# Kernel tuning notes

Hardware: AMD Instinct MI355X
Metric: run time of the kernel (lower is better)

Reference implementation:

```python
import jax, jax.numpy as jnp
import numpy as np

N_NODES = 100000
N_EDGES = 800000
DIM = 64
HEADS = 4
HEAD_DIM = DIM // HEADS  # 16
ALPHA = 0.1
K_ITERS = 8  # fixed-point iterations approximating the implicit/CG solve


def setup_inputs() -> dict:
    key = jax.random.key(0)
    ks = jax.random.split(key, 7)
    x = jax.random.normal(ks[0], (N_NODES, DIM), dtype=jnp.float32)
    edge_index = jax.random.randint(ks[1], (2, N_EDGES), 0, N_NODES, dtype=jnp.int64)
    edge_attr = jax.random.normal(ks[2], (N_EDGES, DIM), dtype=jnp.float32)
    s = 1.0 / np.sqrt(DIM)
    Wq = jax.random.normal(ks[3], (DIM, DIM), dtype=jnp.float32) * s
    Wk = jax.random.normal(ks[4], (DIM, DIM), dtype=jnp.float32) * s
    Wv = jax.random.normal(ks[5], (DIM, DIM), dtype=jnp.float32) * s
    We = jax.random.normal(ks[6], (DIM, DIM), dtype=jnp.float32) * s
    return {"x": x, "edge_index": edge_index, "edge_attr": edge_attr,
            "Wq": Wq, "Wk": Wk, "Wv": Wv, "We": We}


def _mapr(x, edge_index, edge_attr, Wq, Wk, Wv, We):
    N = x.shape[0]
    src, dst = edge_index[0], edge_index[1]
    q = (x @ Wq).reshape(N, HEADS, HEAD_DIM)
    k = (x @ Wk).reshape(N, HEADS, HEAD_DIM)
    v = (x @ Wv).reshape(N, HEADS, HEAD_DIM)
    e = (edge_attr @ We).reshape(-1, HEADS, HEAD_DIM)
    # per-edge multi-head dot attention logits, edge features modulate keys
    logits = jnp.sum(q[dst] * (k[src] + e), axis=-1) / np.sqrt(HEAD_DIM)  # [E,H]
    # segment softmax over incoming edges of each dst node
    m = jax.ops.segment_max(logits, dst, num_segments=N)  # [N,H]
    ex = jnp.exp(logits - m[dst])
    denom = jax.ops.segment_sum(ex, dst, num_segments=N)  # [N,H]
    att = ex / (denom[dst] + 1e-16)  # [E,H]
    # implicit propagation: fixed-point solve of z = alpha*v + (1-alpha) * A_att z
    def step(z, _):
        msg = att[:, :, None] * z[src]                       # [E,H,D]
        agg = jax.ops.segment_sum(msg, dst, num_segments=N)  # [N,H,D]
        return ALPHA * v + (1.0 - ALPHA) * agg, None
    z, _ = jax.lax.scan(step, v, None, length=K_ITERS)
    return z.reshape(N, DIM)


def reference(x, edge_index, edge_attr, Wq, Wk, Wv, We):
    h = _mapr(x, edge_index, edge_attr, Wq, Wk, Wv, We)
    h = jax.nn.relu(h)  # act; dropout is identity in eval mode
    return x + h        # residual
```

## Files before the change

kernel.cpp:

```cpp
#include <hip/hip_runtime.h>
#include <hip/hip_fp16.h>
#include <cstdint>
#include <cstddef>

#define NN 100000
#define NE 800000
#define DIM 64
#define HEADS 4
#define HEAD_DIM 16
#define ALPHA 0.1f
#define K_ITERS 8
#define NBLK 391

typedef short bf16x8 __attribute__((ext_vector_type(8)));
typedef float f32x4 __attribute__((ext_vector_type(4)));
typedef float fvec4 __attribute__((ext_vector_type(4)));

__device__ __forceinline__ unsigned short f2bf(float f) {
    unsigned int x = __float_as_uint(f);
    unsigned int r = (x + 0x7fffu + ((x >> 16) & 1u)) >> 16;
    return (unsigned short)r;
}
__device__ __forceinline__ float bf_lo(unsigned int p) { return __uint_as_float(p << 16); }
__device__ __forceinline__ float bf_hi(unsigned int p) { return __uint_as_float(p & 0xffff0000u); }

__device__ __forceinline__ float2 h2f(unsigned int v) {
    __half2 h = *(__half2*)&v;
    return __half22float2(h);
}
__device__ __forceinline__ unsigned int f2h2(float a, float b) {
    __half2 h = __floats2half2_rn(a, b);
    return *(unsigned int*)&h;
}
__device__ __forceinline__ float dot8h(uint4 a, uint4 b) {
    float2 a0 = h2f(a.x), b0 = h2f(b.x);
    float2 a1 = h2f(a.y), b1 = h2f(b.y);
    float2 a2 = h2f(a.z), b2 = h2f(b.z);
    float2 a3 = h2f(a.w), b3 = h2f(b.w);
    return a0.x * b0.x + a0.y * b0.y + a1.x * b1.x + a1.y * b1.y
         + a2.x * b2.x + a2.y * b2.y + a3.x * b3.x + a3.y * b3.y;
}

#define ACC8(a, V) { float2 t_; \
    t_ = h2f((V).x); m[0] += (a) * t_.x; m[1] += (a) * t_.y; \
    t_ = h2f((V).y); m[2] += (a) * t_.x; m[3] += (a) * t_.y; \
    t_ = h2f((V).z); m[4] += (a) * t_.x; m[5] += (a) * t_.y; \
    t_ = h2f((V).w); m[6] += (a) * t_.x; m[7] += (a) * t_.y; }

__device__ __forceinline__ float rec_att(uint4 r, int head) {
    unsigned int pair = (head & 2) ? r.z : r.y;
    float2 f = h2f(pair);
    return (head & 1) ? f.y : f.x;
}

__global__ __launch_bounds__(256) void qkv_mfma_kernel(
    const float* __restrict__ x,
    const float* __restrict__ Wq, const float* __restrict__ Wk,
    const float* __restrict__ Wv, const float* __restrict__ We,
    __half* __restrict__ qh, __half* __restrict__ kh, __half* __restrict__ vh,
    unsigned short* __restrict__ u)
{
    __shared__ unsigned short sq[64 * 72];
    int tid = threadIdx.x;
    int w = tid >> 6;
    int lane = tid & 63;
    int m16 = lane & 15;
    int quad = lane >> 4;
    int node = blockIdx.x * 64 + w * 16 + m16;
    int nodeC = node < NN ? node : NN - 1;

    bf16x8 afrag[2];
    #pragma unroll
    for (int kk = 0; kk < 2; ++kk) {
        const float* xr = x + (size_t)nodeC * DIM + kk * 32 + quad * 8;
        #pragma unroll
        for (int j = 0; j < 8; ++j) afrag[kk][j] = (short)f2bf(xr[j]);
    }

    const float* Ws[3] = {Wq, Wk, Wv};
    __half* outs[3] = {qh, kh, vh};

    #pragma unroll
    for (int mtx = 0; mtx < 3; ++mtx) {
        const float* W = Ws[mtx];
        #pragma unroll
        for (int n0 = 0; n0 < 64; n0 += 16) {
            int col = n0 + m16;
            f32x4 acc = {0.f, 0.f, 0.f, 0.f};
            #pragma unroll
            for (int kk = 0; kk < 2; ++kk) {
                bf16x8 bfrag;
                #pragma unroll
                for (int j = 0; j < 8; ++j)
                    bfrag[j] = (short)f2bf(W[(kk * 32 + quad * 8 + j) * DIM + col]);
                acc = __builtin_amdgcn_mfma_f32_16x16x32_bf16(afrag[kk], bfrag, acc, 0, 0, 0);
            }
            if (mtx == 0) {
                #pragma unroll
                for (int r = 0; r < 4; ++r) acc[r] *= 0.25f;
            }
            #pragma unroll
            for (int r = 0; r < 4; ++r) {
                int rl = w * 16 + quad * 4 + r;
                int gnode = blockIdx.x * 64 + rl;
                if (mtx == 0) sq[rl * 72 + col] = f2bf(acc[r]);
                if (gnode < NN) outs[mtx][(size_t)gnode * DIM + col] = __float2half(acc[r]);
            }
        }
    }
    __syncthreads();

    #pragma unroll
    for (int h = 0; h < HEADS; ++h) {
        int kk = h >> 1;
        bf16x8 aq;
        const unsigned short* sr = &sq[(w * 16 + m16) * 72 + kk * 32 + quad * 8];
        #pragma unroll
        for (int j = 0; j < 8; ++j) aq[j] = (short)sr[j];
        #pragma unroll
        for (int c0 = 0; c0 < 64; c0 += 16) {
            int c = c0 + m16;
            bf16x8 bfrag;
            #pragma unroll
            for (int j = 0; j < 8; ++j) {
                int k = kk * 32 + quad * 8 + j;
                bfrag[j] = ((k >> 4) == h) ? (short)f2bf(We[c * DIM + k]) : (short)0;
            }
            f32x4 acc = {0.f, 0.f, 0.f, 0.f};
            acc = __builtin_amdgcn_mfma_f32_16x16x32_bf16(aq, bfrag, acc, 0, 0, 0);
            #pragma unroll
            for (int r = 0; r < 4; ++r) {
                int gnode = blockIdx.x * 64 + w * 16 + quad * 4 + r;
                if (gnode < NN) u[(size_t)gnode * 256 + h * 64 + c] = f2bf(acc[r]);
            }
        }
    }
}

__global__ void init_kernel(int* __restrict__ deg) {
    int i = blockIdx.x * 256 + threadIdx.x;
    if (i < NN) deg[i] = 0;
}

__global__ void deg_kernel(const int* __restrict__ ei, int* __restrict__ deg) {
    int e = blockIdx.x * 256 + threadIdx.x;
    if (e >= NE) return;
    atomicAdd(&deg[ei[NE + e]], 1);
}

__global__ void blocksum_kernel(const int* __restrict__ deg, int* __restrict__ bsum) {
    int t = threadIdx.x, b = blockIdx.x;
    int idx = b * 256 + t;
    int v = (idx < NN) ? deg[idx] : 0;
    #pragma unroll
    for (int off = 32; off > 0; off >>= 1) v += __shfl_down(v, off);
    __shared__ int wsum[4];
    if ((t & 63) == 0) wsum[t >> 6] = v;
    __syncthreads();
    if (t == 0) bsum[b] = wsum[0] + wsum[1] + wsum[2] + wsum[3];
}

__global__ void bscan_kernel(const int* __restrict__ bsum, int* __restrict__ boff) {
    __shared__ int s[512];
    int t = threadIdx.x;
    int v = (t < NBLK) ? bsum[t] : 0;
    s[t] = v;
    __syncthreads();
    for (int off = 1; off < 512; off <<= 1) {
        int u = (t >= off) ? s[t - off] : 0;
        __syncthreads();
        s[t] += u;
        __syncthreads();
    }
    if (t < NBLK) boff[t] = s[t] - v;
}

__global__ void rowptr_kernel(const int* __restrict__ deg, const int* __restrict__ boff,
                              int* __restrict__ row_ptr, int* __restrict__ cursor) {
    __shared__ int s[256];
    int t = threadIdx.x, b = blockIdx.x;
    int idx = b * 256 + t;
    int v = (idx < NN) ? deg[idx] : 0;
    s[t] = v;
    __syncthreads();
    for (int off = 1; off < 256; off <<= 1) {
        int u = (t >= off) ? s[t - off] : 0;
        __syncthreads();
        s[t] += u;
        __syncthreads();
    }
    if (idx < NN) {
        int ex = boff[b] + s[t] - v;
        row_ptr[idx] = ex;
        cursor[idx] = ex;
    }
    if (idx == 0) row_ptr[NN] = NE;
}

__global__ void scatter_kernel(const int* __restrict__ ei,
                               int* __restrict__ cursor,
                               int* __restrict__ csr_src,
                               int* __restrict__ csr_e,
                               int* __restrict__ csr_dst) {
    int e = blockIdx.x * 256 + threadIdx.x;
    if (e >= NE) return;
    int src = ei[e], dst = ei[NE + e];
    int pos = atomicAdd(&cursor[dst], 1);
    csr_src[pos] = src;
    csr_e[pos] = e;
    csr_dst[pos] = dst;
}

__global__ __launch_bounds__(256) void logits_edge_kernel(
    const __half* __restrict__ qh,
    const __half* __restrict__ kh,
    const float* __restrict__ edge_attr,
    const unsigned short* __restrict__ u,
    const int* __restrict__ ei,
    __half* __restrict__ att_e) {
    int idx = blockIdx.x * 256 + threadIdx.x;
    if (idx >= NE * HEADS) return;
    int e = idx >> 2, h = idx & 3;
    int src = ei[e], dst = ei[NE + e];
    const fvec4* attr4 = (const fvec4*)edge_attr + (size_t)e * 16;
    const uint4* u4 = (const uint4*)u + (size_t)dst * 32 + h * 8;
    float au = 0.f;
    #pragma unroll
    for (int i = 0; i < 8; ++i) {
        uint4 up = u4[i];
        fvec4 a0 = __builtin_nontemporal_load(attr4 + 2 * i);
        fvec4 a1 = __builtin_nontemporal_load(attr4 + 2 * i + 1);
        au += a0.x * bf_lo(up.x) + a0.y * bf_hi(up.x)
            + a0.z * bf_lo(up.y) + a0.w * bf_hi(up.y)
            + a1.x * bf_lo(up.z) + a1.y * bf_hi(up.z)
            + a1.z * bf_lo(up.w) + a1.w * bf_hi(up.w);
    }
    const uint4* qq = (const uint4*)qh + (size_t)dst * 8 + h * 2;
    const uint4* kk = (const uint4*)kh + (size_t)src * 8 + h * 2;
    float qk = dot8h(qq[0], kk[0]) + dot8h(qq[1], kk[1]);
    float ex = __expf(qk + au);
    att_e[idx] = __float2half(ex);
}

__global__ void rinv_kernel(const __half* __restrict__ att_e,
                            const int* __restrict__ csr_e,
                            const int* __restrict__ row_ptr,
                            float* __restrict__ rinv) {
    int idx = blockIdx.x * 256 + threadIdx.x;
    if (idx >= NN * HEADS) return;
    int n = idx >> 2, h = idx & 3;
    int beg = row_ptr[n], end = row_ptr[n + 1];
    float s = 0.f;
    int j = beg;
    for (; j + 2 <= end; j += 2) {
        int e0 = csr_e[j], e1 = csr_e[j + 1];
        float a0 = __half2float(att_e[e0 * 4 + h]);
        float a1 = __half2float(att_e[e1 * 4 + h]);
        s += a0 + a1;
    }
    if (j < end) s += __half2float(att_e[csr_e[j] * 4 + h]);
    rinv[idx] = 0.9f / (s + 1e-16f);
}

__global__ void recs_kernel(const __half* __restrict__ att_e,
                            const int* __restrict__ csr_src,
                            const int* __restrict__ csr_e,
                            const int* __restrict__ csr_dst,
                            const float* __restrict__ rinv,
                            uint4* __restrict__ recs) {
    int j = blockIdx.x * 256 + threadIdx.x;
    if (j >= NE) return;
    int e = csr_e[j], src = csr_src[j], dst = csr_dst[j];
    uint2 ap = *(const uint2*)(att_e + (size_t)e * 4);
    float2 e01 = h2f(ap.x), e23 = h2f(ap.y);
    float4 rv = *(const float4*)(rinv + (size_t)dst * 4);
    uint4 rec;
    rec.x = (unsigned int)src;
    rec.y = f2h2(e01.x * rv.x, e01.y * rv.y);
    rec.z = f2h2(e23.x * rv.z, e23.y * rv.w);
    rec.w = 0u;
    recs[j] = rec;
}

__global__ __launch_bounds__(256) void prop_rec_kernel(
    const __half* __restrict__ zin,
    const __half* __restrict__ vh,
    const uint4* __restrict__ recs,
    const int* __restrict__ row_ptr,
    __half* __restrict__ zout) {
    int gid = blockIdx.x * 256 + threadIdx.x;
    int node = gid >> 3;
    if (node >= NN) return;
    int l = gid & 7;
    int head = l >> 1;
    const uint4* z4 = (const uint4*)zin;
    float m[8];
    #pragma unroll
    for (int i = 0; i < 8; ++i) m[i] = 0.f;
    int beg = row_ptr[node], end = row_ptr[node + 1];
    int j = beg;
    for (; j + 4 <= end; j += 4) {
        uint4 r0 = recs[j], r1 = recs[j + 1], r2 = recs[j + 2], r3 = recs[j + 3];
        uint4 z0 = z4[(size_t)r0.x * 8 + l];
        uint4 z1 = z4[(size_t)r1.x * 8 + l];
        uint4 z2 = z4[(size_t)r2.x * 8 + l];
        uint4 z3 = z4[(size_t)r3.x * 8 + l];
        float a0 = rec_att(r0, head), a1 = rec_att(r1, head);
        float a2 = rec_att(r2, head), a3 = rec_att(r3, head);
        ACC8(a0, z0); ACC8(a1, z1); ACC8(a2, z2); ACC8(a3, z3);
    }
    for (; j < end; ++j) {
        uint4 r = recs[j];
        uint4 zl = z4[(size_t)r.x * 8 + l];
        float a = rec_att(r, head);
        ACC8(a, zl);
    }
    uint4 vv = ((const uint4*)vh)[(size_t)node * 8 + l];
    float2 v0 = h2f(vv.x), v1 = h2f(vv.y), v2 = h2f(vv.z), v3 = h2f(vv.w);
    uint4 o;
    o.x = f2h2(ALPHA * v0.x + m[0], ALPHA * v0.y + m[1]);
    o.y = f2h2(ALPHA * v1.x + m[2], ALPHA * v1.y + m[3]);
    o.z = f2h2(ALPHA * v2.x + m[4], ALPHA * v2.y + m[5]);
    o.w = f2h2(ALPHA * v3.x + m[6], ALPHA * v3.y + m[7]);
    ((uint4*)zout)[(size_t)node * 8 + l] = o;
}

__global__ __launch_bounds__(256) void prop_out_rec_kernel(
    const __half* __restrict__ zin,
    const __half* __restrict__ vh,
    const uint4* __restrict__ recs,
    const int* __restrict__ row_ptr,
    const float* __restrict__ x,
    float* __restrict__ out) {
    int gid = blockIdx.x * 256 + threadIdx.x;
    int node = gid >> 3;
    if (node >= NN) return;
    int l = gid & 7;
    int head = l >> 1;
    const uint4* z4 = (const uint4*)zin;
    float m[8];
    #pragma unroll
    for (int i = 0; i < 8; ++i) m[i] = 0.f;
    int beg = row_ptr[node], end = row_ptr[node + 1];
    int j = beg;
    for (; j + 4 <= end; j += 4) {
        uint4 r0 = recs[j], r1 = recs[j + 1], r2 = recs[j + 2], r3 = recs[j + 3];
        uint4 z0 = z4[(size_t)r0.x * 8 + l];
        uint4 z1 = z4[(size_t)r1.x * 8 + l];
        uint4 z2 = z4[(size_t)r2.x * 8 + l];
        uint4 z3 = z4[(size_t)r3.x * 8 + l];
        float a0 = rec_att(r0, head), a1 = rec_att(r1, head);
        float a2 = rec_att(r2, head), a3 = rec_att(r3, head);
        ACC8(a0, z0); ACC8(a1, z1); ACC8(a2, z2); ACC8(a3, z3);
    }
    for (; j < end; ++j) {
        uint4 r = recs[j];
        uint4 zl = z4[(size_t)r.x * 8 + l];
        float a = rec_att(r, head);
        ACC8(a, zl);
    }
    uint4 vv = ((const uint4*)vh)[(size_t)node * 8 + l];
    float2 v0 = h2f(vv.x), v1 = h2f(vv.y), v2 = h2f(vv.z), v3 = h2f(vv.w);
    float zf[8] = { ALPHA * v0.x + m[0], ALPHA * v0.y + m[1],
                    ALPHA * v1.x + m[2], ALPHA * v1.y + m[3],
                    ALPHA * v2.x + m[4], ALPHA * v2.y + m[5],
                    ALPHA * v3.x + m[6], ALPHA * v3.y + m[7] };
    const float4* x4 = (const float4*)x + (size_t)node * 16 + l * 2;
    float4 xa = x4[0], xb = x4[1];
    float4 oa, ob;
    oa.x = xa.x + fmaxf(zf[0], 0.f); oa.y = xa.y + fmaxf(zf[1], 0.f);
    oa.z = xa.z + fmaxf(zf[2], 0.f); oa.w = xa.w + fmaxf(zf[3], 0.f);
    ob.x = xb.x + fmaxf(zf[4], 0.f); ob.y = xb.y + fmaxf(zf[5], 0.f);
    ob.z = xb.z + fmaxf(zf[6], 0.f); ob.w = xb.w + fmaxf(zf[7], 0.f);
    float4* o4 = (float4*)out + (size_t)node * 16 + l * 2;
    o4[0] = oa; o4[1] = ob;
}

extern "C" void kernel_launch(void* const* d_in, const int* in_sizes, int n_in,
                              void* d_out, int out_size, void* d_ws, size_t ws_size,
                              hipStream_t stream) {
    const float* x         = (const float*)d_in[0];
    const int*   ei        = (const int*)d_in[1];
    const float* edge_attr = (const float*)d_in[2];
    const float* Wq        = (const float*)d_in[3];
    const float* Wk        = (const float*)d_in[4];
    const float* Wv        = (const float*)d_in[5];
    const float* We        = (const float*)d_in[6];
    float* out = (float*)d_out;

    __half* qh = (__half*)d_ws;
    __half* kh = qh + (size_t)NN * DIM;
    __half* vh = kh + (size_t)NN * DIM;
    unsigned short* u = (unsigned short*)(vh + (size_t)NN * DIM);
    __half* zha = (__half*)(u + (size_t)NN * 256);
    __half* zhb = zha + (size_t)NN * DIM;
    __half* att_e = zhb + (size_t)NN * DIM;
    float* rinv  = (float*)(att_e + (size_t)NE * HEADS);
    uint4* recs  = (uint4*)(rinv + (size_t)NN * HEADS);
    int* deg     = (int*)(recs + (size_t)NE);
    int* bsum    = deg + NN;
    int* boff    = bsum + NBLK;
    int* row_ptr = boff + NBLK;
    int* cursor  = row_ptr + NN + 1;
    int* csr_src = cursor + NN;
    int* csr_e   = csr_src + NE;
    int* csr_dst = csr_e + NE;

    hipLaunchKernelGGL(qkv_mfma_kernel, dim3((NN + 63) / 64), dim3(256), 0, stream,
                       x, Wq, Wk, Wv, We, qh, kh, vh, u);
    hipLaunchKernelGGL(init_kernel, dim3((NN + 255) / 256), dim3(256), 0, stream,
                       deg);
    hipLaunchKernelGGL(deg_kernel, dim3((NE + 255) / 256), dim3(256), 0, stream,
                       ei, deg);
    hipLaunchKernelGGL(blocksum_kernel, dim3(NBLK), dim3(256), 0, stream,
                       deg, bsum);
    hipLaunchKernelGGL(bscan_kernel, dim3(1), dim3(512), 0, stream,
                       bsum, boff);
    hipLaunchKernelGGL(rowptr_kernel, dim3(NBLK), dim3(256), 0, stream,
                       deg, boff, row_ptr, cursor);
    hipLaunchKernelGGL(scatter_kernel, dim3((NE + 255) / 256), dim3(256), 0, stream,
                       ei, cursor, csr_src, csr_e, csr_dst);
    hipLaunchKernelGGL(logits_edge_kernel, dim3(NE * HEADS / 256), dim3(256), 0, stream,
                       qh, kh, edge_attr, u, ei, att_e);
    hipLaunchKernelGGL(rinv_kernel, dim3((NN * HEADS + 255) / 256), dim3(256), 0, stream,
                       att_e, csr_e, row_ptr, rinv);
    hipLaunchKernelGGL(recs_kernel, dim3((NE + 255) / 256), dim3(256), 0, stream,
                       att_e, csr_src, csr_e, csr_dst, rinv, recs);

    const __half* zin = vh;
    __half* zout = zha;
    for (int it = 0; it < K_ITERS - 1; ++it) {
        hipLaunchKernelGGL(prop_rec_kernel, dim3((NN * 8 + 255) / 256), dim3(256), 0, stream,
                           zin, vh, recs, row_ptr, zout);
        zin = zout;
        zout = (zout == zha) ? zhb : zha;
    }
    hipLaunchKernelGGL(prop_out_rec_kernel, dim3((NN * 8 + 255) / 256), dim3(256), 0, stream,
                       zin, vh, recs, row_ptr, x, out);
}
```

Before: 847.4 us.

## Compute logits in CSR order per edge, fuse softmax normalization, deepen prop unroll

The logits kernel now runs one thread per edge in CSR order and handles all four heads, writing attention packed per CSR slot. This removes the scattered csr_e indirection when later summing. The separate rinv and recs kernels are merged into one per-node kernel that sums and then normalizes in two passes over contiguous entries. The propagation kernels also gain an 8-wide unrolled gather loop for more memory-level parallelism. The trade-offs are reading edge_attr in CSR order, which is a random gather, and higher register pressure from the deeper unroll.

Measured after the change: 800.6 us. 5.5% less time.

```diff
diff --git a/kernel.cpp b/kernel.cpp
--- a/kernel.cpp
+++ b/kernel.cpp
@@ -39,6 +39,12 @@
     float2 a3 = h2f(a.w), b3 = h2f(b.w);
     return a0.x * b0.x + a0.y * b0.y + a1.x * b1.x + a1.y * b1.y
          + a2.x * b2.x + a2.y * b2.y + a3.x * b3.x + a3.y * b3.y;
+}
+__device__ __forceinline__ float dot8bf(fvec4 a0, fvec4 a1, uint4 up) {
+    return a0.x * bf_lo(up.x) + a0.y * bf_hi(up.x)
+         + a0.z * bf_lo(up.y) + a0.w * bf_hi(up.y)
+         + a1.x * bf_lo(up.z) + a1.y * bf_hi(up.z)
+         + a1.z * bf_lo(up.w) + a1.w * bf_hi(up.w);
 }
 
 #define ACC8(a, V) { float2 t_; \
@@ -211,75 +217,70 @@
     csr_dst[pos] = dst;
 }
 
-__global__ __launch_bounds__(256) void logits_edge_kernel(
+__global__ __launch_bounds__(256) void logits_csr2_kernel(
     const __half* __restrict__ qh,
     const __half* __restrict__ kh,
     const float* __restrict__ edge_attr,
     const unsigned short* __restrict__ u,
-    const int* __restrict__ ei,
-    __half* __restrict__ att_e) {
-    int idx = blockIdx.x * 256 + threadIdx.x;
-    if (idx >= NE * HEADS) return;
-    int e = idx >> 2, h = idx & 3;
-    int src = ei[e], dst = ei[NE + e];
+    const int* __restrict__ csr_src,
+    const int* __restrict__ csr_e,
+    const int* __restrict__ csr_dst,
+    uint2* __restrict__ att) {
+    int j = blockIdx.x * 256 + threadIdx.x;
+    if (j >= NE) return;
+    int src = csr_src[j], dst = csr_dst[j], e = csr_e[j];
     const fvec4* attr4 = (const fvec4*)edge_attr + (size_t)e * 16;
-    const uint4* u4 = (const uint4*)u + (size_t)dst * 32 + h * 8;
-    float au = 0.f;
+    const uint4* urow = (const uint4*)u + (size_t)dst * 32;
+    float au0 = 0.f, au1 = 0.f, au2 = 0.f, au3 = 0.f;
     #pragma unroll
     for (int i = 0; i < 8; ++i) {
-        uint4 up = u4[i];
         fvec4 a0 = __builtin_nontemporal_load(attr4 + 2 * i);
         fvec4 a1 = __builtin_nontemporal_load(attr4 + 2 * i + 1);
-        au += a0.x * bf_lo(up.x) + a0.y * bf_hi(up.x)
-            + a0.z * bf_lo(up.y) + a0.w * bf_hi(up.y)
-            + a1.x * bf_lo(up.z) + a1.y * bf_hi(up.z)
-            + a1.z * bf_lo(up.w) + a1.w * bf_hi(up.w);
-    }
-    const uint4* qq = (const uint4*)qh + (size_t)dst * 8 + h * 2;
-    const uint4* kk = (const uint4*)kh + (size_t)src * 8 + h * 2;
-    float qk = dot8h(qq[0], kk[0]) + dot8h(qq[1], kk[1]);
-    float ex = __expf(qk + au);
-    att_e[idx] = __float2half(ex);
-}
-
-__global__ void rinv_kernel(const __half* __restrict__ att_e,
-                            const int* __restrict__ csr_e,
-                            const int* __restrict__ row_ptr,
-                            float* __restrict__ rinv) {
-    int idx = blockIdx.x * 256 + threadIdx.x;
-    if (idx >= NN * HEADS) return;
-    int n = idx >> 2, h = idx & 3;
+        au0 += dot8bf(a0, a1, urow[0 * 8 + i]);
+        au1 += dot8bf(a0, a1, urow[1 * 8 + i]);
+        au2 += dot8bf(a0, a1, urow[2 * 8 + i]);
+        au3 += dot8bf(a0, a1, urow[3 * 8 + i]);
+    }
+    const uint4* qq = (const uint4*)qh + (size_t)dst * 8;
+    const uint4* kk = (const uint4*)kh + (size_t)src * 8;
+    float qk0 = dot8h(qq[0], kk[0]) + dot8h(qq[1], kk[1]);
+    float qk1 = dot8h(qq[2], kk[2]) + dot8h(qq[3], kk[3]);
+    float qk2 = dot8h(qq[4], kk[4]) + dot8h(qq[5], kk[5]);
+    float qk3 = dot8h(qq[6], kk[6]) + dot8h(qq[7], kk[7]);
+    float e0 = __expf(qk0 + au0);
+    float e1 = __expf(qk1 + au1);
+    float e2 = __expf(qk2 + au2);
+    float e3 = __expf(qk3 + au3);
+    uint2 o;
+    o.x = f2h2(e0, e1);
+    o.y = f2h2(e2, e3);
+    att[j] = o;
+}
+
+__global__ void recs_fused_kernel(const uint2* __restrict__ att,
+                                  const int* __restrict__ csr_src,
+                                  const int* __restrict__ row_ptr,
+                                  uint4* __restrict__ recs) {
+    int n = blockIdx.x * 256 + threadIdx.x;
+    if (n >= NN) return;
     int beg = row_ptr[n], end = row_ptr[n + 1];
-    float s = 0.f;
-    int j = beg;
-    for (; j + 2 <= end; j += 2) {
-        int e0 = csr_e[j], e1 = csr_e[j + 1];
-        float a0 = __half2float(att_e[e0 * 4 + h]);
-        float a1 = __half2float(att_e[e1 * 4 + h]);
-        s += a0 + a1;
-    }
-    if (j < end) s += __half2float(att_e[csr_e[j] * 4 + h]);
-    rinv[idx] = 0.9f / (s + 1e-16f);
-}
-
-__global__ void recs_kernel(const __half* __restrict__ att_e,
-                            const int* __restrict__ csr_src,
-                            const int* __restrict__ csr_e,
-                            const int* __restrict__ csr_dst,
-                            const float* __restrict__ rinv,
-                            uint4* __restrict__ recs) {
-    int j = blockIdx.x * 256 + threadIdx.x;
-    if (j >= NE) return;
-    int e = csr_e[j], src = csr_src[j], dst = csr_dst[j];
-    uint2 ap = *(const uint2*)(att_e + (size_t)e * 4);
-    float2 e01 = h2f(ap.x), e23 = h2f(ap.y);
-    float4 rv = *(const float4*)(rinv + (size_t)dst * 4);
-    uint4 rec;
-    rec.x = (unsigned int)src;
-    rec.y = f2h2(e01.x * rv.x, e01.y * rv.y);
-    rec.z = f2h2(e23.x * rv.z, e23.y * rv.w);
-    rec.w = 0u;
-    recs[j] = rec;
+    float s0 = 1e-16f, s1 = 1e-16f, s2 = 1e-16f, s3 = 1e-16f;
+    for (int j = beg; j < end; ++j) {
+        uint2 ap = att[j];
+        float2 p01 = h2f(ap.x), p23 = h2f(ap.y);
+        s0 += p01.x; s1 += p01.y; s2 += p23.x; s3 += p23.y;
+    }
+    float r0 = 0.9f / s0, r1 = 0.9f / s1, r2 = 0.9f / s2, r3 = 0.9f / s3;
+    for (int j = beg; j < end; ++j) {
+        uint2 ap = att[j];
+        float2 p01 = h2f(ap.x), p23 = h2f(ap.y);
+        uint4 rec;
+        rec.x = (unsigned int)csr_src[j];
+        rec.y = f2h2(p01.x * r0, p01.y * r1);
+        rec.z = f2h2(p23.x * r2, p23.y * r3);
+        rec.w = 0u;
+        recs[j] = rec;
+    }
 }
 
 __global__ __launch_bounds__(256) void prop_rec_kernel(
@@ -299,6 +300,15 @@
     for (int i = 0; i < 8; ++i) m[i] = 0.f;
     int beg = row_ptr[node], end = row_ptr[node + 1];
     int j = beg;
+    for (; j + 8 <= end; j += 8) {
+        uint4 r[8], zz[8];
+        #pragma unroll
+        for (int t = 0; t < 8; ++t) r[t] = recs[j + t];
+        #pragma unroll
+        for (int t = 0; t < 8; ++t) zz[t] = z4[(size_t)r[t].x * 8 + l];
+        #pragma unroll
+        for (int t = 0; t < 8; ++t) { float a = rec_att(r[t], head); ACC8(a, zz[t]); }
+    }
     for (; j + 4 <= end; j += 4) {
         uint4 r0 = recs[j], r1 = recs[j + 1], r2 = recs[j + 2], r3 = recs[j + 3];
         uint4 z0 = z4[(size_t)r0.x * 8 + l];
@@ -343,6 +353,15 @@
     for (int i = 0; i < 8; ++i) m[i] = 0.f;
     int beg = row_ptr[node], end = row_ptr[node + 1];
     int j = beg;
+    for (; j + 8 <= end; j += 8) {
+        uint4 r[8], zz[8];
+        #pragma unroll
+        for (int t = 0; t < 8; ++t) r[t] = recs[j + t];
+        #pragma unroll
+        for (int t = 0; t < 8; ++t) zz[t] = z4[(size_t)r[t].x * 8 + l];
+        #pragma unroll
+        for (int t = 0; t < 8; ++t) { float a = rec_att(r[t], head); ACC8(a, zz[t]); }
+    }
     for (; j + 4 <= end; j += 4) {
         uint4 r0 = recs[j], r1 = recs[j + 1], r2 = recs[j + 2], r3 = recs[j + 3];
         uint4 z0 = z4[(size_t)r0.x * 8 + l];
@@ -394,9 +413,8 @@
     unsigned short* u = (unsigned short*)(vh + (size_t)NN * DIM);
     __half* zha = (__half*)(u + (size_t)NN * 256);
     __half* zhb = zha + (size_t)NN * DIM;
-    __half* att_e = zhb + (size_t)NN * DIM;
-    float* rinv  = (float*)(att_e + (size_t)NE * HEADS);
-    uint4* recs  = (uint4*)(rinv + (size_t)NN * HEADS);
+    uint2* att   = (uint2*)(zhb + (size_t)NN * DIM);
+    uint4* recs  = (uint4*)(att + (size_t)NE);
     int* deg     = (int*)(recs + (size_t)NE);
     int* bsum    = deg + NN;
     int* boff    = bsum + NBLK;
@@ -420,12 +438,10 @@
                        deg, boff, row_ptr, cursor);
     hipLaunchKernelGGL(scatter_kernel, dim3((NE + 255) / 256), dim3(256), 0, stream,
                        ei, cursor, csr_src, csr_e, csr_dst);
-    hipLaunchKernelGGL(logits_edge_kernel, dim3(NE * HEADS / 256), dim3(256), 0, stream,
-                       qh, kh, edge_attr, u, ei, att_e);
-    hipLaunchKernelGGL(rinv_kernel, dim3((NN * HEADS + 255) / 256), dim3(256), 0, stream,
-                       att_e, csr_e, row_ptr, rinv);
-    hipLaunchKernelGGL(recs_kernel, dim3((NE + 255) / 256), dim3(256), 0, stream,
-                       att_e, csr_src, csr_e, csr_dst, rinv, recs);
+    hipLaunchKernelGGL(logits_csr2_kernel, dim3((NE + 255) / 256), dim3(256), 0, stream,
+                       qh, kh, edge_attr, u, csr_src, csr_e, csr_dst, att);
+    hipLaunchKernelGGL(recs_fused_kernel, dim3((NN + 255) / 256), dim3(256), 0, stream,
+                       att, csr_src, row_ptr, recs);
 
     const __half* zin = vh;
     __half* zout = zha;
```
